# Performance work log

Measured on AMD Instinct MI355X. Metric: run time of the kernel, lower is better.

The kernel has to match this reference:

```python
import jax, jax.numpy as jnp
import numpy as np

EPS = 1e-6
N_HEADS, N_KV = 16, 4


def rmsnorm(x, w):
    return x * jax.lax.rsqrt(jnp.mean(x * x, axis=-1, keepdims=True) + EPS) * w


def setup_inputs() -> dict:
    key = jax.random.key(0)
    ks = jax.random.split(key, 9)
    B, T, D, F = 2, 2048, 2048, 8192
    KVD = N_KV * (D // N_HEADS)
    s = lambda k, shape, fan: (jax.random.normal(k, shape, jnp.float32) * (fan ** -0.5))
    return {
        "x": jax.random.normal(ks[0], (B, T, D), jnp.float32),
        "norm1_w": jnp.ones((D,), jnp.float32),
        "norm2_w": jnp.ones((D,), jnp.float32),
        "Wq": s(ks[1], (D, D), D),
        "Wk": s(ks[2], (D, KVD), D),
        "Wv": s(ks[3], (D, KVD), D),
        "Wo": s(ks[4], (D, D), D),
        "Wc": s(ks[5], (D, D), D),
        "W1": s(ks[6], (D, F), D),
        "W2": s(ks[7], (F, D), F),
        "W3": s(ks[8], (D, F), D),
    }


def reference(x, norm1_w, norm2_w, Wq, Wk, Wv, Wo, Wc, W1, W2, W3):
    B, T, D = x.shape
    dh = D // N_HEADS          # 128
    G = N_HEADS // N_KV        # groups per kv head
    scale = dh ** -0.5

    xn = rmsnorm(x, norm1_w)
    q = xn @ Wq                               # [B,T,D]
    pos = q @ Wc                              # CoPE stand-in: contextual positional bias on Q
    q = (q + pos).reshape(B, T, N_KV, G, dh)  # group q heads under their kv head
    k = (xn @ Wk).reshape(B, T, N_KV, dh)
    v = (xn @ Wv).reshape(B, T, N_KV, dh)

    # GQA without repeat_interleave: contract each group against shared K/V
    scores = jnp.einsum('bqkgd,bskd->bkgqs', q, k) * scale   # [B,KV,G,T,T]
    i = jnp.arange(T)
    causal = i[:, None] >= i[None, :]
    scores = jnp.where(causal, scores, -jnp.inf)
    w = jax.nn.softmax(scores, axis=-1)
    att = jnp.einsum('bkgqs,bskd->bqkgd', w, v).reshape(B, T, D)

    x = x + att @ Wo
    xn2 = rmsnorm(x, norm2_w)
    x = x + (jax.nn.silu(xn2 @ W1) * (xn2 @ W3)) @ W2
    return x
```

## Files before the change

kernel.cpp:

```cpp
#include <hip/hip_runtime.h>
#include <hip/hip_bf16.h>

typedef __attribute__((ext_vector_type(8))) short short8;
typedef __attribute__((ext_vector_type(4))) float floatx4;
typedef unsigned short ushort_t;

__device__ inline float b2f(ushort_t s) {
    return __uint_as_float(((unsigned int)s) << 16);
}
__device__ inline ushort_t f2b(float f) {
    unsigned int u = __float_as_uint(f);
    unsigned int r = 0x7fff + ((u >> 16) & 1);
    return (ushort_t)((u + r) >> 16);
}
__device__ inline void load8(const float* p, float* f) {
    float4 a = *(const float4*)p;
    float4 b = *(const float4*)(p + 4);
    f[0] = a.x; f[1] = a.y; f[2] = a.z; f[3] = a.w;
    f[4] = b.x; f[5] = b.y; f[6] = b.z; f[7] = b.w;
}
__device__ inline void gload16(const ushort_t* g, ushort_t* l) {
    __builtin_amdgcn_global_load_lds(
        (const __attribute__((address_space(1))) unsigned int*)g,
        (__attribute__((address_space(3))) unsigned int*)l, 16, 0, 0);
}

__global__ __launch_bounds__(256) void transpose_all(
    const float* __restrict__ s0, const float* __restrict__ s1,
    const float* __restrict__ s2, const float* __restrict__ s3,
    const float* __restrict__ s4, const float* __restrict__ s5,
    const float* __restrict__ s6, const float* __restrict__ s7,
    ushort_t* d0, ushort_t* d1, ushort_t* d2, ushort_t* d3,
    ushort_t* d4, ushort_t* d5, ushort_t* d6, ushort_t* d7) {
    int id = blockIdx.x;
    const float* src; ushort_t* dst; int K, N;
    if (id < 1024)       { src = s0; dst = d0; K = 2048; N = 2048; }
    else if (id < 1280)  { id -= 1024;  src = s1; dst = d1; K = 2048; N = 512; }
    else if (id < 1536)  { id -= 1280;  src = s2; dst = d2; K = 2048; N = 512; }
    else if (id < 2560)  { id -= 1536;  src = s3; dst = d3; K = 2048; N = 2048; }
    else if (id < 3584)  { id -= 2560;  src = s4; dst = d4; K = 2048; N = 2048; }
    else if (id < 7680)  { id -= 3584;  src = s5; dst = d5; K = 2048; N = 8192; }
    else if (id < 11776) { id -= 7680;  src = s6; dst = d6; K = 2048; N = 8192; }
    else                 { id -= 11776; src = s7; dst = d7; K = 8192; N = 2048; }
    int tn = N >> 6;
    int kb = (id / tn) * 64, nb = (id % tn) * 64;
    __shared__ ushort_t tile[64][65];
    int t = threadIdx.x;
#pragma unroll
    for (int i = 0; i < 4; ++i) {
        int r = (t >> 4) + i * 16;
        int c = (t & 15) * 4;
        float4 v = *(const float4*)(src + (size_t)(kb + r) * N + nb + c);
        tile[c + 0][r] = f2b(v.x);
        tile[c + 1][r] = f2b(v.y);
        tile[c + 2][r] = f2b(v.z);
        tile[c + 3][r] = f2b(v.w);
    }
    __syncthreads();
#pragma unroll
    for (int i = 0; i < 2; ++i) {
        int s = t + i * 256;
        int n = s >> 3, kc = (s & 7) * 8;
        ushort_t o[8];
#pragma unroll
        for (int j = 0; j < 8; ++j) o[j] = tile[n][kc + j];
        *(uint4*)(dst + (size_t)(nb + n) * K + kb + kc) = *(const uint4*)o;
    }
}

__global__ __launch_bounds__(256) void rmsnorm_kernel(const float* __restrict__ x,
                                                      const float* __restrict__ w,
                                                      ushort_t* __restrict__ out, int D) {
    int row = blockIdx.x;
    int t = threadIdx.x;
    const float* xr = x + (size_t)row * D;
    float f[8];
    load8(xr + t * 8, f);
    float ss = 0.f;
#pragma unroll
    for (int i = 0; i < 8; ++i) ss += f[i] * f[i];
#pragma unroll
    for (int m = 1; m < 64; m <<= 1) ss += __shfl_xor(ss, m);
    __shared__ float wsum[4];
    if ((t & 63) == 0) wsum[t >> 6] = ss;
    __syncthreads();
    float tot = wsum[0] + wsum[1] + wsum[2] + wsum[3];
    float r = rsqrtf(tot / (float)D + 1e-6f);
    float wf[8];
    load8(w + t * 8, wf);
    ushort_t o[8];
#pragma unroll
    for (int i = 0; i < 8; ++i) o[i] = f2b(f[i] * r * wf[i]);
    *(uint4*)(out + (size_t)row * D + t * 8) = *(const uint4*)o;
}

__global__ __launch_bounds__(256) void reduce_out(const ushort_t* __restrict__ p,
                                                  const float* __restrict__ resid,
                                                  float* __restrict__ out, int n) {
    int stride = gridDim.x * 256;
    for (int i = blockIdx.x * 256 + threadIdx.x; i * 8 < n; i += stride) {
        int i8 = i * 8;
        uint4 a = *(const uint4*)(p + i8);
        uint4 b = *(const uint4*)(p + n + i8);
        const ushort_t* ae = (const ushort_t*)&a;
        const ushort_t* be = (const ushort_t*)&b;
        float rr[8];
        load8(resid + i8, rr);
        float o[8];
#pragma unroll
        for (int j = 0; j < 8; ++j) o[j] = b2f(ae[j]) + b2f(be[j]) + rr[j];
        *(float4*)(out + i8) = make_float4(o[0], o[1], o[2], o[3]);
        *(float4*)(out + i8 + 4) = make_float4(o[4], o[5], o[6], o[7]);
    }
}

__device__ inline void vm6() { asm volatile("s_waitcnt vmcnt(6)" ::: "memory"); }
__device__ inline void vm4() { asm volatile("s_waitcnt vmcnt(4)" ::: "memory"); }

template <int MODE>
__global__ __launch_bounds__(512, 2) void gemm8(const ushort_t* __restrict__ A,
                                                const ushort_t* __restrict__ Bt,
                                                const ushort_t* __restrict__ aux,
                                                const float* __restrict__ aux2,
                                                void* __restrict__ Cv,
                                                void* __restrict__ C2v,
                                                void* __restrict__ C3v,
                                                int M, int N, int Ksub, int lda) {
    __shared__ __align__(16) ushort_t Lds[2 * 32768];
    const int tid = threadIdx.x;
    const int wv = tid >> 6, lane = tid & 63;
    const int l16 = lane & 15, l4 = lane >> 4;
    const int wr = wv >> 2, wc = wv & 3;
    int nwg = gridDim.x;
    int per = nwg >> 3;
    int wg = (blockIdx.x & 7) * per + (blockIdx.x >> 3);
    int mtiles = M >> 8;
    int bx = wg & (mtiles - 1);
    int by = wg / mtiles;
    int bm = bx << 8, bn = by << 8;
    int koff = blockIdx.y * Ksub;

    const int sr = tid >> 3;
    const int scol = (((tid & 7) ^ (sr & 7)) << 3);
    const ushort_t* gA = A + (size_t)(bm + sr) * lda + scol + koff;
    const ushort_t* gB = Bt + (size_t)(bn + sr) * lda + scol + koff;
    ushort_t* ldsw = Lds + wv * 512;

    const int ktiles = Ksub >> 6;
    const int niter = ktiles >> 1;
    const int km = ktiles - 1;

#define STG_A(slot, j, kt) gload16(gA + (size_t)((j) * 64) * lda + ((kt) << 6), ldsw + (slot) * 32768 + (j) * 4096)
#define STG_B(slot, j, kt) gload16(gB + (size_t)((j) * 64) * lda + ((kt) << 6), ldsw + (slot) * 32768 + 16384 + (j) * 4096)

    STG_A(0, 0, 0); STG_A(0, 2, 0); STG_A(0, 1, 0); STG_A(0, 3, 0);
    STG_B(0, 0, 0); STG_B(0, 1, 0); STG_B(0, 2, 0); STG_B(0, 3, 0);
    STG_A(1, 0, 1); STG_A(1, 2, 1);
    STG_B(1, 0, 1); STG_B(1, 1, 1); STG_B(1, 2, 1); STG_B(1, 3, 1);
    vm6();
    asm volatile("" ::: "memory");
    __builtin_amdgcn_s_barrier();

    const int lx = l4 ^ (l16 & 7);
    floatx4 acc[8][4] = {};
    short8 aR[4][2], bR[4][2];

#define DSA(slot, mh) { _Pragma("unroll") for (int m = 0; m < 4; ++m) { \
    _Pragma("unroll") for (int kk = 0; kk < 2; ++kk) \
      aR[m][kk] = *(const short8*)(Lds + (slot) * 32768 + \
          (wr * 128 + (mh) * 64 + m * 16 + l16) * 64 + ((lx ^ (kk << 2)) << 3)); } }
#define DSB(slot, nh) { _Pragma("unroll") for (int n = 0; n < 2; ++n) { \
    _Pragma("unroll") for (int kk = 0; kk < 2; ++kk) \
      bR[(nh) * 2 + n][kk] = *(const short8*)(Lds + (slot) * 32768 + 16384 + \
          (wc * 64 + ((nh) * 2 + n) * 16 + l16) * 64 + ((lx ^ (kk << 2)) << 3)); } }
#define QUAD(mh, nlo) { _Pragma("unroll") for (int m = 0; m < 4; ++m) \
    _Pragma("unroll") for (int n = 0; n < 2; ++n) \
    _Pragma("unroll") for (int kk = 0; kk < 2; ++kk) \
      acc[(mh) * 4 + m][(nlo) + n] = __builtin_amdgcn_mfma_f32_16x16x32_bf16( \
          aR[m][kk], bR[(nlo) + n][kk], acc[(mh) * 4 + m][(nlo) + n], 0, 0, 0); }
#define PHASE(DS, ST, MH, NLO, VM) { \
    DS; ST; \
    asm volatile("" ::: "memory"); \
    __builtin_amdgcn_s_barrier(); \
    asm volatile("s_waitcnt lgkmcnt(0)" ::: "memory"); \
    __builtin_amdgcn_sched_barrier(0); \
    __builtin_amdgcn_s_setprio(1); \
    QUAD(MH, NLO); \
    __builtin_amdgcn_s_setprio(0); \
    VM; \
    asm volatile("" ::: "memory"); \
    __builtin_amdgcn_s_barrier(); }

    for (int it = 0; it < niter; ++it) {
        int t1 = 2 * it + 1;
        int t2 = (2 * it + 2) & km;
        int t3 = (2 * it + 3) & km;
        PHASE({ DSA(0, 0); DSB(0, 0); }, { STG_A(1, 1, t1); STG_A(1, 3, t1); }, 0, 0, );
        PHASE({ DSB(0, 1); },            { STG_A(0, 0, t2); STG_A(0, 2, t2); }, 0, 2, );
        PHASE({ DSA(0, 1); },            { STG_B(0, 0, t2); STG_B(0, 1, t2); }, 1, 2, );
        PHASE({ },                       { STG_B(0, 2, t2); STG_B(0, 3, t2); }, 1, 0, vm6(); );
        PHASE({ DSA(1, 0); DSB(1, 0); }, { STG_A(0, 1, t2); STG_A(0, 3, t2); }, 0, 0, );
        PHASE({ DSB(1, 1); },            { STG_A(1, 0, t3); STG_A(1, 2, t3); }, 0, 2, );
        PHASE({ DSA(1, 1); },            { STG_B(1, 0, t3); STG_B(1, 1, t3); }, 1, 2, );
        PHASE({ },                       { STG_B(1, 2, t3); STG_B(1, 3, t3); }, 1, 0, vm6(); );
    }

#pragma unroll
    for (int mi = 0; mi < 8; ++mi)
#pragma unroll
        for (int ni = 0; ni < 4; ++ni)
#pragma unroll
            for (int r = 0; r < 4; ++r) {
                int row = bm + wr * 128 + mi * 16 + l4 * 4 + r;
                int col = bn + wc * 64 + ni * 16 + l16;
                size_t idx = (size_t)row * N + col;
                float v = acc[mi][ni][r];
                if (MODE == 0) {
                    ((ushort_t*)Cv)[idx] = f2b(v);
                } else if (MODE == 1) {
                    ((ushort_t*)Cv)[idx] = f2b(v + b2f(aux[idx]));
                } else if (MODE == 2) {
                    float h = b2f(aux[idx]);
                    ((ushort_t*)Cv)[idx] = f2b((h / (1.f + __expf(-h))) * v);
                } else if (MODE == 3) {
                    ((ushort_t*)Cv)[(size_t)blockIdx.y * M * N + idx] = f2b(v);
                } else if (MODE == 5) {
                    ((float*)Cv)[idx] = v + aux2[idx];
                } else if (MODE == 6) {
                    if (bn < 2048) {
                        ((ushort_t*)Cv)[(size_t)row * 2048 + col] = f2b(v);
                    } else if (bn < 2560) {
                        ((ushort_t*)C2v)[(size_t)row * 512 + (col - 2048)] = f2b(v);
                    } else {
                        ((ushort_t*)C3v)[(size_t)(col - 2560) * 4096 + row] = f2b(v);
                    }
                }
            }
#undef STG_A
#undef STG_B
#undef DSA
#undef DSB
#undef QUAD
#undef PHASE
}

template <int MODE>
__global__ __launch_bounds__(512, 1) void gemm8h(const ushort_t* __restrict__ A,
                                                 const ushort_t* __restrict__ Bt,
                                                 const ushort_t* __restrict__ aux,
                                                 const float* __restrict__ aux2,
                                                 void* __restrict__ Cv,
                                                 int M, int N, int K) {
    __shared__ __align__(16) ushort_t Lds[2 * 24576];
    const int tid = threadIdx.x;
    const int wv = tid >> 6, lane = tid & 63;
    const int l16 = lane & 15, l4 = lane >> 4;
    const int wr = wv >> 2, wc = wv & 3;
    int nwg = gridDim.x;
    int per = nwg >> 3;
    int wg = (blockIdx.x & 7) * per + (blockIdx.x >> 3);
    int mtiles = M >> 7;
    int bx = wg & (mtiles - 1);
    int by = wg / mtiles;
    int bm = bx << 7, bn = by << 8;

    const int sr = tid >> 3;
    const int scol = (((tid & 7) ^ (sr & 7)) << 3);
    const ushort_t* gA = A + (size_t)(bm + sr) * K + scol;
    const ushort_t* gB = Bt + (size_t)(bn + sr) * K + scol;
    ushort_t* ldsw = Lds + wv * 512;

    const int ktiles = K >> 6;
    const int niter = ktiles >> 1;
    const int km = ktiles - 1;

#define HSTG_A(slot, j, kt) gload16(gA + (size_t)((j) * 64) * K + ((kt) << 6), ldsw + (slot) * 24576 + (j) * 4096)
#define HSTG_B(slot, j, kt) gload16(gB + (size_t)((j) * 64) * K + ((kt) << 6), ldsw + (slot) * 24576 + 8192 + (j) * 4096)

    HSTG_A(0, 0, 0); HSTG_A(0, 1, 0);
    HSTG_B(0, 0, 0); HSTG_B(0, 1, 0); HSTG_B(0, 2, 0); HSTG_B(0, 3, 0);
    HSTG_A(1, 0, 1); HSTG_A(1, 1, 1);
    HSTG_B(1, 0, 1); HSTG_B(1, 1, 1);
    vm4();
    asm volatile("" ::: "memory");
    __builtin_amdgcn_s_barrier();

    const int lx = l4 ^ (l16 & 7);
    floatx4 acc[4][4] = {};
    short8 aR[2][2], bR[4][2];

#define HDSA(slot, mh) { _Pragma("unroll") for (int m = 0; m < 2; ++m) { \
    _Pragma("unroll") for (int kk = 0; kk < 2; ++kk) \
      aR[m][kk] = *(const short8*)(Lds + (slot) * 24576 + \
          (wr * 64 + (mh) * 32 + m * 16 + l16) * 64 + ((lx ^ (kk << 2)) << 3)); } }
#define HDSB(slot, nh) { _Pragma("unroll") for (int n = 0; n < 2; ++n) { \
    _Pragma("unroll") for (int kk = 0; kk < 2; ++kk) \
      bR[(nh) * 2 + n][kk] = *(const short8*)(Lds + (slot) * 24576 + 8192 + \
          (wc * 64 + ((nh) * 2 + n) * 16 + l16) * 64 + ((lx ^ (kk << 2)) << 3)); } }
#define HQUAD(mh, nlo) { _Pragma("unroll") for (int m = 0; m < 2; ++m) \
    _Pragma("unroll") for (int n = 0; n < 2; ++n) \
    _Pragma("unroll") for (int kk = 0; kk < 2; ++kk) \
      acc[(mh) * 2 + m][(nlo) + n] = __builtin_amdgcn_mfma_f32_16x16x32_bf16( \
          aR[m][kk], bR[(nlo) + n][kk], acc[(mh) * 2 + m][(nlo) + n], 0, 0, 0); }
#define HPHASE(DS, ST, MH, NLO, VM) { \
    DS; ST; \
    asm volatile("" ::: "memory"); \
    __builtin_amdgcn_s_barrier(); \
    asm volatile("s_waitcnt lgkmcnt(0)" ::: "memory"); \
    __builtin_amdgcn_sched_barrier(0); \
    __builtin_amdgcn_s_setprio(1); \
    HQUAD(MH, NLO); \
    __builtin_amdgcn_s_setprio(0); \
    VM; \
    asm volatile("" ::: "memory"); \
    __builtin_amdgcn_s_barrier(); }

    for (int it = 0; it < niter; ++it) {
        int t1 = 2 * it + 1;
        int t2 = (2 * it + 2) & km;
        int t3 = (2 * it + 3) & km;
        HPHASE({ HDSA(0, 0); HDSB(0, 0); }, { HSTG_B(1, 2, t1); HSTG_B(1, 3, t1); }, 0, 0, );
        HPHASE({ HDSB(0, 1); },             { },                                     0, 2, );
        HPHASE({ HDSA(0, 1); },             { HSTG_B(0, 0, t2); HSTG_B(0, 1, t2); }, 1, 2, );
        HPHASE({ },                         { HSTG_B(0, 2, t2); HSTG_B(0, 3, t2); }, 1, 0, vm4(); );
        HPHASE({ HDSA(1, 0); HDSB(1, 0); }, { HSTG_A(0, 0, t2); HSTG_A(0, 1, t2); }, 0, 0, );
        HPHASE({ HDSB(1, 1); },             { },                                     0, 2, );
        HPHASE({ HDSA(1, 1); },             { HSTG_B(1, 0, t3); HSTG_B(1, 1, t3); }, 1, 2, );
        HPHASE({ },                         { HSTG_A(1, 0, t3); HSTG_A(1, 1, t3); }, 1, 0, vm4(); );
    }

#pragma unroll
    for (int mi = 0; mi < 4; ++mi)
#pragma unroll
        for (int ni = 0; ni < 4; ++ni)
#pragma unroll
            for (int r = 0; r < 4; ++r) {
                int row = bm + wr * 64 + mi * 16 + l4 * 4 + r;
                int col = bn + wc * 64 + ni * 16 + l16;
                size_t idx = (size_t)row * N + col;
                float v = acc[mi][ni][r];
                if (MODE == 1) ((ushort_t*)Cv)[idx] = f2b(v + b2f(aux[idx]));
                else if (MODE == 5) ((float*)Cv)[idx] = v + aux2[idx];
            }
#undef HSTG_A
#undef HSTG_B
#undef HDSA
#undef HDSB
#undef HQUAD
#undef HPHASE
}

#define QB 64
#define SB 64

__global__ __launch_bounds__(256, 2) void attn_kernel(const ushort_t* __restrict__ Q,
                                                      const ushort_t* __restrict__ Kb,
                                                      const ushort_t* __restrict__ VbT,
                                                      ushort_t* __restrict__ O, int Tlen) {
    const int D = 2048, KVD = 512, dh = 128;
    const int MTOK = 4096;
    int p = blockIdx.x, h = blockIdx.y, b = blockIdx.z;
    int kv = h >> 2;
    int t = threadIdx.x, wave = t >> 6, lane = t & 63;
    int l16 = lane & 15, l4 = lane >> 4;
    __shared__ __align__(16) ushort_t Ks[2][SB][dh + 8];
    __shared__ __align__(16) ushort_t Vt[2][dh][SB + 8];
    __shared__ __align__(16) ushort_t Ps[4][16][SB + 8];
    const float scale = 0.08838834764831845f;
    const ushort_t* Kg = Kb + ((size_t)(b * Tlen) + (t >> 4)) * KVD + kv * dh + (t & 15) * 8;
    const ushort_t* Vg = VbT + (size_t)(kv * dh + (t >> 3)) * MTOK + b * Tlen + (t & 7) * 8;

    for (int side = 0; side < 2; ++side) {
        int qt = side ? p : (31 - p);
        int qbase = qt * QB;
        int qfrag = qbase + wave * 16;
        short8 qf[4];
        const ushort_t* Qrow = Q + ((size_t)(b * Tlen) + qfrag + l16) * D + h * dh;
#pragma unroll
        for (int kk = 0; kk < 4; ++kk) qf[kk] = *(const short8*)(Qrow + kk * 32 + l4 * 8);
        floatx4 o_acc[8] = {};
        float m_r[4], l_r[4];
#pragma unroll
        for (int r = 0; r < 4; ++r) { m_r[r] = -INFINITY; l_r[r] = 0.f; }
        int nst = qt + 1;
        uint4 kreg[4], vreg[4];
#pragma unroll
        for (int p4 = 0; p4 < 4; ++p4) {
            kreg[p4] = *(const uint4*)(Kg + (size_t)(p4 * 16) * KVD);
            vreg[p4] = *(const uint4*)(Vg + (size_t)(p4 * 32) * MTOK);
        }
        __syncthreads();
#pragma unroll
        for (int p4 = 0; p4 < 4; ++p4) {
            *(uint4*)(&Ks[0][(t >> 4) + p4 * 16][(t & 15) * 8]) = kreg[p4];
            *(uint4*)(&Vt[0][(t >> 3) + p4 * 32][(t & 7) * 8]) = vreg[p4];
        }
        if (nst > 1) {
#pragma unroll
            for (int p4 = 0; p4 < 4; ++p4) {
                kreg[p4] = *(const uint4*)(Kg + (size_t)(SB + p4 * 16) * KVD);
                vreg[p4] = *(const uint4*)(Vg + (size_t)(p4 * 32) * MTOK + SB);
            }
        }
        __syncthreads();
        for (int st = 0; st < nst; ++st) {
            int cur = st & 1;
            int s0 = st * SB;
            floatx4 sa[4] = {};
            __builtin_amdgcn_s_setprio(1);
#pragma unroll
            for (int ss = 0; ss < 4; ++ss)
#pragma unroll
                for (int kk = 0; kk < 4; ++kk) {
                    short8 kf = *(const short8*)(&Ks[cur][ss * 16 + l16][kk * 32 + l4 * 8]);
                    sa[ss] = __builtin_amdgcn_mfma_f32_16x16x32_bf16(qf[kk], kf, sa[ss], 0, 0, 0);
                }
            __builtin_amdgcn_s_setprio(0);
            if (st + 1 < nst) {
#pragma unroll
                for (int p4 = 0; p4 < 4; ++p4) {
                    *(uint4*)(&Ks[cur ^ 1][(t >> 4) + p4 * 16][(t & 15) * 8]) = kreg[p4];
                    *(uint4*)(&Vt[cur ^ 1][(t >> 3) + p4 * 32][(t & 7) * 8]) = vreg[p4];
                }
            }
            if (st + 2 < nst) {
                size_t off = (size_t)(st + 2) * SB;
#pragma unroll
                for (int p4 = 0; p4 < 4; ++p4) {
                    kreg[p4] = *(const uint4*)(Kg + (off + p4 * 16) * KVD);
                    vreg[p4] = *(const uint4*)(Vg + (size_t)(p4 * 32) * MTOK + off);
                }
            }
            float sv[4][4], pmax[4];
#pragma unroll
            for (int r = 0; r < 4; ++r) pmax[r] = -INFINITY;
#pragma unroll
            for (int ss = 0; ss < 4; ++ss) {
                int scol = s0 + ss * 16 + l16;
#pragma unroll
                for (int r = 0; r < 4; ++r) {
                    int qrow = qfrag + l4 * 4 + r;
                    float v = sa[ss][r] * scale;
                    if (scol > qrow) v = -INFINITY;
                    sv[ss][r] = v;
                    pmax[r] = fmaxf(pmax[r], v);
                }
            }
#pragma unroll
            for (int m = 1; m < 16; m <<= 1)
#pragma unroll
                for (int r = 0; r < 4; ++r) pmax[r] = fmaxf(pmax[r], __shfl_xor(pmax[r], m));
            int cflag = 1;
#pragma unroll
            for (int r = 0; r < 4; ++r) cflag &= (pmax[r] <= m_r[r] + 8.f) ? 1 : 0;
            bool skip = __all(cflag);
            float mn[4], rsum[4];
#pragma unroll
            for (int r = 0; r < 4; ++r) {
                mn[r] = skip ? m_r[r] : fmaxf(m_r[r], pmax[r]);
                rsum[r] = 0.f;
            }
#pragma unroll
            for (int ss = 0; ss < 4; ++ss)
#pragma unroll
                for (int r = 0; r < 4; ++r) {
                    float pv = __expf(sv[ss][r] - mn[r]);
                    sv[ss][r] = pv;
                    rsum[r] += pv;
                }
#pragma unroll
            for (int m = 1; m < 16; m <<= 1)
#pragma unroll
                for (int r = 0; r < 4; ++r) rsum[r] += __shfl_xor(rsum[r], m);
            if (skip) {
#pragma unroll
                for (int r = 0; r < 4; ++r) l_r[r] += rsum[r];
            } else {
#pragma unroll
                for (int r = 0; r < 4; ++r) {
                    float esc = __expf(m_r[r] - mn[r]);
                    l_r[r] = l_r[r] * esc + rsum[r];
                    m_r[r] = mn[r];
#pragma unroll
                    for (int c = 0; c < 8; ++c) o_acc[c][r] *= esc;
                }
            }
#pragma unroll
            for (int ss = 0; ss < 4; ++ss)
#pragma unroll
                for (int r = 0; r < 4; ++r)
                    Ps[wave][l4 * 4 + r][ss * 16 + l16] = f2b(sv[ss][r]);
            short8 pa[2];
#pragma unroll
            for (int kk = 0; kk < 2; ++kk)
                pa[kk] = *(const short8*)(&Ps[wave][l16][kk * 32 + l4 * 8]);
            __builtin_amdgcn_s_setprio(1);
#pragma unroll
            for (int c = 0; c < 8; ++c)
#pragma unroll
                for (int kk = 0; kk < 2; ++kk) {
                    short8 vf = *(const short8*)(&Vt[cur][c * 16 + l16][kk * 32 + l4 * 8]);
                    o_acc[c] = __builtin_amdgcn_mfma_f32_16x16x32_bf16(pa[kk], vf, o_acc[c], 0, 0, 0);
                }
            __builtin_amdgcn_s_setprio(0);
            __syncthreads();
        }
        ushort_t* Osh = &Ks[0][0][0];
#pragma unroll
        for (int c = 0; c < 8; ++c)
#pragma unroll
            for (int r = 0; r < 4; ++r)
                Osh[(wave * 16 + l4 * 4 + r) * 136 + c * 16 + l16] = f2b(o_acc[c][r] / l_r[r]);
        __syncthreads();
        {
            int orow = t >> 2, occ = (t & 3) * 32;
            const ushort_t* srcp = Osh + orow * 136 + occ;
            ushort_t* dstp = O + ((size_t)(b * Tlen) + qbase + orow) * D + h * dh + occ;
#pragma unroll
            for (int k = 0; k < 4; ++k)
                *(uint4*)(dstp + k * 8) = *(const uint4*)(srcp + k * 8);
        }
    }
}

extern "C" void kernel_launch(void* const* d_in, const int* in_sizes, int n_in,
                              void* d_out, int out_size, void* d_ws, size_t ws_size,
                              hipStream_t stream) {
    const float* x   = (const float*)d_in[0];
    const float* n1w = (const float*)d_in[1];
    const float* n2w = (const float*)d_in[2];
    const float* Wq  = (const float*)d_in[3];
    const float* Wk  = (const float*)d_in[4];
    const float* Wv  = (const float*)d_in[5];
    const float* Wo  = (const float*)d_in[6];
    const float* Wc  = (const float*)d_in[7];
    const float* W1  = (const float*)d_in[8];
    const float* W2  = (const float*)d_in[9];
    const float* W3  = (const float*)d_in[10];
    float* out = (float*)d_out;

    const int B = 2, T = 2048, D = 2048, F = 8192, KVD = 512;
    const int M = B * T;
    const size_t XD   = (size_t)M * D * 2;
    const size_t XDF  = (size_t)M * D * 4;
    const size_t KVSZ = (size_t)M * KVD * 2;
    const size_t MF   = (size_t)M * F * 2;
    const size_t WDD  = (size_t)D * D * 2;
    const size_t WQKV = (size_t)(D + 2 * KVD) * D * 2;
    const size_t WDF  = (size_t)D * F * 2;

    char* w = (char*)d_ws;
    ushort_t* xn    = (ushort_t*)(w);
    ushort_t* qtmp  = (ushort_t*)(w + XD);
    ushort_t* qfin  = (ushort_t*)(w + 2 * XD);
    float*    x2f   = (float*)   (w + 3 * XD);
    ushort_t* kbuf  = (ushort_t*)(w + 3 * XD + XDF);
    ushort_t* vbufT = (ushort_t*)(w + 3 * XD + XDF + KVSZ);
    ushort_t* h1    = (ushort_t*)(w + 3 * XD + XDF + 2 * KVSZ);
    char* wt = w + 3 * XD + XDF + 2 * KVSZ + MF;
    ushort_t* WqkvT = (ushort_t*)(wt);
    ushort_t* WcT   = (ushort_t*)(wt + WQKV);
    ushort_t* WoT   = (ushort_t*)(wt + WQKV + WDD);
    ushort_t* W1T   = (ushort_t*)(wt + WQKV + 2 * WDD);
    ushort_t* W3T   = (ushort_t*)(wt + WQKV + 2 * WDD + WDF);
    ushort_t* W2T   = (ushort_t*)(wt + WQKV + 2 * WDD + 2 * WDF);

    dim3 blk(256);
    dim3 blk8(512);

    transpose_all<<<15872, blk, 0, stream>>>(
        Wq, Wk, Wv, Wc, Wo, W1, W3, W2,
        WqkvT, WqkvT + (size_t)2048 * D, WqkvT + (size_t)2560 * D,
        WcT, WoT, W1T, W3T, W2T);

    rmsnorm_kernel<<<M, blk, 0, stream>>>(x, n1w, xn, D);
    gemm8<6><<<dim3((M / 256) * (3072 / 256)), blk8, 0, stream>>>(
        xn, WqkvT, nullptr, nullptr, qtmp, kbuf, vbufT, M, 3072, D, D);
    gemm8h<1><<<dim3((M / 128) * (D / 256)), blk8, 0, stream>>>(
        qtmp, WcT, qtmp, nullptr, qfin, M, D, D);
    attn_kernel<<<dim3(16, 16, B), blk, 0, stream>>>(qfin, kbuf, vbufT, qtmp, T);
    gemm8h<5><<<dim3((M / 128) * (D / 256)), blk8, 0, stream>>>(
        qtmp, WoT, nullptr, x, x2f, M, D, D);
    rmsnorm_kernel<<<M, blk, 0, stream>>>(x2f, n2w, xn, D);
    gemm8<0><<<dim3((M / 256) * (F / 256)), blk8, 0, stream>>>(
        xn, W1T, nullptr, nullptr, h1, nullptr, nullptr, M, F, D, D);
    gemm8<2><<<dim3((M / 256) * (F / 256)), blk8, 0, stream>>>(
        xn, W3T, h1, nullptr, h1, nullptr, nullptr, M, F, D, D);
    gemm8<3><<<dim3((M / 256) * (D / 256), 2), blk8, 0, stream>>>(
        h1, W2T, nullptr, nullptr, xn, nullptr, nullptr, M, D, F / 2, F);
    reduce_out<<<1024, blk, 0, stream>>>(xn, x2f, out, M * D);
}
```

Measured before the change: 810.3 us.

## Transpose score MFMA so each lane owns one query row in softmax

Swaps the MFMA operands for QK^T so the score tile comes out transposed, with each lane holding one query column and key rows spread over its registers. Row max and sum then need only two cross-lane shuffles instead of four rounds for each of four rows, and each lane keeps a single running max and sum. P is packed to bf16 with a paired convert instruction and stored as 32-bit words, and the final normalisation uses reciprocals fetched by shuffle. The rescale and finish steps now need extra __shfl broadcasts to map per-query stats back onto the accumulator layout.

```diff
diff --git a/kernel.cpp b/kernel.cpp
--- a/kernel.cpp
+++ b/kernel.cpp
@@ -12,6 +12,11 @@
     unsigned int u = __float_as_uint(f);
     unsigned int r = 0x7fff + ((u >> 16) & 1);
     return (ushort_t)((u + r) >> 16);
+}
+__device__ inline unsigned int cvtpk(float lo, float hi) {
+    unsigned int r;
+    asm("v_cvt_pk_bf16_f32 %0, %1, %2" : "=v"(r) : "v"(lo), "v"(hi));
+    return r;
 }
 __device__ inline void load8(const float* p, float* f) {
     float4 a = *(const float4*)p;
@@ -365,7 +370,7 @@
     int l16 = lane & 15, l4 = lane >> 4;
     __shared__ __align__(16) ushort_t Ks[2][SB][dh + 8];
     __shared__ __align__(16) ushort_t Vt[2][dh][SB + 8];
-    __shared__ __align__(16) ushort_t Ps[4][16][SB + 8];
+    __shared__ __align__(16) unsigned int Ps2[4][16][36];
     const float scale = 0.08838834764831845f;
     const ushort_t* Kg = Kb + ((size_t)(b * Tlen) + (t >> 4)) * KVD + kv * dh + (t & 15) * 8;
     const ushort_t* Vg = VbT + (size_t)(kv * dh + (t >> 3)) * MTOK + b * Tlen + (t & 7) * 8;
@@ -374,14 +379,13 @@
         int qt = side ? p : (31 - p);
         int qbase = qt * QB;
         int qfrag = qbase + wave * 16;
+        int qcol = qfrag + l16;
         short8 qf[4];
         const ushort_t* Qrow = Q + ((size_t)(b * Tlen) + qfrag + l16) * D + h * dh;
 #pragma unroll
         for (int kk = 0; kk < 4; ++kk) qf[kk] = *(const short8*)(Qrow + kk * 32 + l4 * 8);
         floatx4 o_acc[8] = {};
-        float m_r[4], l_r[4];
-#pragma unroll
-        for (int r = 0; r < 4; ++r) { m_r[r] = -INFINITY; l_r[r] = 0.f; }
+        float m_s = -INFINITY, l_s = 0.f;
         int nst = qt + 1;
         uint4 kreg[4], vreg[4];
 #pragma unroll
@@ -413,7 +417,7 @@
 #pragma unroll
                 for (int kk = 0; kk < 4; ++kk) {
                     short8 kf = *(const short8*)(&Ks[cur][ss * 16 + l16][kk * 32 + l4 * 8]);
-                    sa[ss] = __builtin_amdgcn_mfma_f32_16x16x32_bf16(qf[kk], kf, sa[ss], 0, 0, 0);
+                    sa[ss] = __builtin_amdgcn_mfma_f32_16x16x32_bf16(kf, qf[kk], sa[ss], 0, 0, 0);
                 }
             __builtin_amdgcn_s_setprio(0);
             if (st + 1 < nst) {
@@ -431,69 +435,60 @@
                     vreg[p4] = *(const uint4*)(Vg + (size_t)(p4 * 32) * MTOK + off);
                 }
             }
-            float sv[4][4], pmax[4];
-#pragma unroll
-            for (int r = 0; r < 4; ++r) pmax[r] = -INFINITY;
+            float sv[4][4];
+            float pmax = -INFINITY;
+#pragma unroll
+            for (int ss = 0; ss < 4; ++ss)
+#pragma unroll
+                for (int r = 0; r < 4; ++r) {
+                    int krow = s0 + ss * 16 + l4 * 4 + r;
+                    float v = sa[ss][r] * scale;
+                    if (krow > qcol) v = -INFINITY;
+                    sv[ss][r] = v;
+                    pmax = fmaxf(pmax, v);
+                }
+            pmax = fmaxf(pmax, __shfl_xor(pmax, 16));
+            pmax = fmaxf(pmax, __shfl_xor(pmax, 32));
+            bool skip = __all(pmax <= m_s + 8.f);
+            float mn = skip ? m_s : fmaxf(m_s, pmax);
+            float rsum = 0.f;
+#pragma unroll
+            for (int ss = 0; ss < 4; ++ss)
+#pragma unroll
+                for (int r = 0; r < 4; ++r) {
+                    float pv = __expf(sv[ss][r] - mn);
+                    sv[ss][r] = pv;
+                    rsum += pv;
+                }
+            rsum += __shfl_xor(rsum, 16);
+            rsum += __shfl_xor(rsum, 32);
+            if (skip) {
+                l_s += rsum;
+            } else {
+                float esc = __expf(m_s - mn);
+                l_s = l_s * esc + rsum;
+                m_s = mn;
+                float ef[4];
+#pragma unroll
+                for (int r = 0; r < 4; ++r) ef[r] = __shfl(esc, l4 * 4 + r);
+#pragma unroll
+                for (int c = 0; c < 8; ++c)
+#pragma unroll
+                    for (int r = 0; r < 4; ++r) o_acc[c][r] *= ef[r];
+            }
 #pragma unroll
             for (int ss = 0; ss < 4; ++ss) {
-                int scol = s0 + ss * 16 + l16;
-#pragma unroll
-                for (int r = 0; r < 4; ++r) {
-                    int qrow = qfrag + l4 * 4 + r;
-                    float v = sa[ss][r] * scale;
-                    if (scol > qrow) v = -INFINITY;
-                    sv[ss][r] = v;
-                    pmax[r] = fmaxf(pmax[r], v);
-                }
-            }
-#pragma unroll
-            for (int m = 1; m < 16; m <<= 1)
-#pragma unroll
-                for (int r = 0; r < 4; ++r) pmax[r] = fmaxf(pmax[r], __shfl_xor(pmax[r], m));
-            int cflag = 1;
-#pragma unroll
-            for (int r = 0; r < 4; ++r) cflag &= (pmax[r] <= m_r[r] + 8.f) ? 1 : 0;
-            bool skip = __all(cflag);
-            float mn[4], rsum[4];
-#pragma unroll
-            for (int r = 0; r < 4; ++r) {
-                mn[r] = skip ? m_r[r] : fmaxf(m_r[r], pmax[r]);
-                rsum[r] = 0.f;
-            }
-#pragma unroll
-            for (int ss = 0; ss < 4; ++ss)
-#pragma unroll
-                for (int r = 0; r < 4; ++r) {
-                    float pv = __expf(sv[ss][r] - mn[r]);
-                    sv[ss][r] = pv;
-                    rsum[r] += pv;
-                }
-#pragma unroll
-            for (int m = 1; m < 16; m <<= 1)
-#pragma unroll
-                for (int r = 0; r < 4; ++r) rsum[r] += __shfl_xor(rsum[r], m);
-            if (skip) {
-#pragma unroll
-                for (int r = 0; r < 4; ++r) l_r[r] += rsum[r];
-            } else {
-#pragma unroll
-                for (int r = 0; r < 4; ++r) {
-                    float esc = __expf(m_r[r] - mn[r]);
-                    l_r[r] = l_r[r] * esc + rsum[r];
-                    m_r[r] = mn[r];
-#pragma unroll
-                    for (int c = 0; c < 8; ++c) o_acc[c][r] *= esc;
-                }
-            }
-#pragma unroll
-            for (int ss = 0; ss < 4; ++ss)
-#pragma unroll
-                for (int r = 0; r < 4; ++r)
-                    Ps[wave][l4 * 4 + r][ss * 16 + l16] = f2b(sv[ss][r]);
+                uint2 pk;
+                pk.x = cvtpk(sv[ss][0], sv[ss][1]);
+                pk.y = cvtpk(sv[ss][2], sv[ss][3]);
+                *(uint2*)&Ps2[wave][l16][ss * 8 + l4 * 2] = pk;
+            }
             short8 pa[2];
 #pragma unroll
-            for (int kk = 0; kk < 2; ++kk)
-                pa[kk] = *(const short8*)(&Ps[wave][l16][kk * 32 + l4 * 8]);
+            for (int kk = 0; kk < 2; ++kk) {
+                uint4 pv4 = *(const uint4*)&Ps2[wave][l16][kk * 16 + l4 * 4];
+                pa[kk] = *(const short8*)&pv4;
+            }
             __builtin_amdgcn_s_setprio(1);
 #pragma unroll
             for (int c = 0; c < 8; ++c)
@@ -505,12 +500,15 @@
             __builtin_amdgcn_s_setprio(0);
             __syncthreads();
         }
+        float linv[4];
+#pragma unroll
+        for (int r = 0; r < 4; ++r) linv[r] = 1.f / __shfl(l_s, l4 * 4 + r);
         ushort_t* Osh = &Ks[0][0][0];
 #pragma unroll
         for (int c = 0; c < 8; ++c)
 #pragma unroll
             for (int r = 0; r < 4; ++r)
-                Osh[(wave * 16 + l4 * 4 + r) * 136 + c * 16 + l16] = f2b(o_acc[c][r] / l_r[r]);
+                Osh[(wave * 16 + l4 * 4 + r) * 136 + c * 16 + l16] = f2b(o_acc[c][r] * linv[r]);
         __syncthreads();
         {
             int orow = t >> 2, occ = (t & 3) * 32;
```

Result: no change. 795.8 us (-1.8%).
